# Optimization experiments

Hardware: AMD Instinct MI355X
Metric: run time of the kernel (lower is better)

Reference implementation:

```python
import jax, jax.numpy as jnp
import numpy as np

# Production-scale perfect decision-tree ensemble (Hummingbird perf_tree_trav layout)
B, F, T, D, C = 16384, 256, 512, 7, 4  # batch, features, trees, internal levels below root, classes


def setup_inputs() -> dict:
    key = jax.random.key(0)
    k = jax.random.split(key, 6)
    total = T * (2 ** (D + 1) - 2)  # concatenated per-level node/bias tables, level l has T*2^l entries
    return {
        "x": jax.random.normal(k[0], (B, F), dtype=jnp.float32),
        "root_nodes": jax.random.randint(k[1], (T,), 0, F, dtype=jnp.int32),
        "root_biases": jax.random.normal(k[2], (T,), dtype=jnp.float32),
        "tree_indices": jnp.arange(T, dtype=jnp.int32) * 2,
        "nodes_flat": jax.random.randint(k[3], (total,), 0, F, dtype=jnp.int32),
        "biases_flat": jax.random.normal(k[4], (total,), dtype=jnp.float32),
        "leaf_nodes": jax.random.normal(k[5], (T * 2 ** (D + 1), C), dtype=jnp.float32),
    }


def reference(x, root_nodes, root_biases, tree_indices, nodes_flat, biases_flat, leaf_nodes):
    # Root level: compare each tree's root feature against its bias. decision_cond = less (lt).
    # tree_indices = t*2 offsets indices into the flat level-1 table of size 2T;
    # the offset doubles along with the level size via `2*idx + cond`.
    idx = (x[:, root_nodes] < root_biases).astype(jnp.int32) + tree_indices  # [B, T]
    off = 0
    for l in range(1, D + 1):  # static loop over tree depth
        size = T << l
        lvl_nodes = nodes_flat[off:off + size]
        lvl_biases = biases_flat[off:off + size]
        feat_idx = lvl_nodes[idx]                          # [B, T] feature ids for current nodes
        feats = jnp.take_along_axis(x, feat_idx, axis=1)   # [B, T] per-sample feature gather
        idx = 2 * idx + (feats < lvl_biases[idx]).astype(jnp.int32)
        off += size
    leaves = leaf_nodes[idx]                               # [B, T, C]
    return leaves.sum(axis=1)                              # [B, C]
```

## Files before the change

### kernel.cpp

```cpp
#include <hip/hip_runtime.h>

#define BB 16384
#define FF 256
#define TT 512
#define DD 7

constexpr int S_  = 64;
constexpr int NT_ = 1024;
constexpr int NTG = NT_ / S_;
constexpr int HT  = TT / 2;
constexpr int TPT = HT / NTG;
constexpr int NP  = 8;
constexpr int NJ  = TPT / NP;

constexpr int NR1 = TT * 2;
constexpr int NR3 = TT * 8;
constexpr int NR5 = TT * 32;
constexpr int NN7 = TT * 128;
constexpr int NRECS = NR1 + NR3 + NR5 + NN7;

constexpr size_t OFF_R3   = (size_t)NR1 * 16;
constexpr size_t OFF_R5   = OFF_R3 + (size_t)NR3 * 16;
constexpr size_t OFF_N7   = OFF_R5 + (size_t)NR5 * 16;
constexpr size_t OFF_PART = OFF_N7 + (size_t)NN7 * 8;
constexpr size_t WS_NEED  = OFF_PART + (size_t)2 * BB * 4 * sizeof(float);

__global__ void pack_kernel(const int* __restrict__ nf, const float* __restrict__ bf,
                            int4* __restrict__ R1, int4* __restrict__ R3,
                            int4* __restrict__ R5, int2* __restrict__ N7) {
    const int i = blockIdx.x * 256 + threadIdx.x;
    if (i < NR1) {
        const int e0 = i, eC = 2 * TT + 2 * i;
        const int fp = (nf[e0] & 255) | ((nf[eC] & 255) << 8) | ((nf[eC + 1] & 255) << 16);
        R1[i] = make_int4(fp, __float_as_int(bf[e0]),
                          __float_as_int(bf[eC]), __float_as_int(bf[eC + 1]));
    } else if (i < NR1 + NR3) {
        const int r = i - NR1;
        const int e0 = 6 * TT + r, eC = 14 * TT + 2 * r;
        const int fp = (nf[e0] & 255) | ((nf[eC] & 255) << 8) | ((nf[eC + 1] & 255) << 16);
        R3[r] = make_int4(fp, __float_as_int(bf[e0]),
                          __float_as_int(bf[eC]), __float_as_int(bf[eC + 1]));
    } else if (i < NR1 + NR3 + NR5) {
        const int r = i - NR1 - NR3;
        const int e0 = 30 * TT + r, eC = 62 * TT + 2 * r;
        const int fp = (nf[e0] & 255) | ((nf[eC] & 255) << 8) | ((nf[eC + 1] & 255) << 16);
        R5[r] = make_int4(fp, __float_as_int(bf[e0]),
                          __float_as_int(bf[eC]), __float_as_int(bf[eC + 1]));
    } else if (i < NRECS) {
        const int r = i - NR1 - NR3 - NR5;
        const int e = 126 * TT + r;
        N7[r] = make_int2(nf[e], __float_as_int(bf[e]));
    }
}

__device__ __forceinline__ int step2(const int4 w, const int i,
                                     const float* __restrict__ x_s,
                                     const int xb, const int sz) {
    const float v0 = x_s[xb | ((w.x & 255) ^ sz)];
    const float vL = x_s[xb | (((w.x >> 8) & 255) ^ sz)];
    const float vR = x_s[xb | (((w.x >> 16) & 255) ^ sz)];
    const int   c0 = (v0 < __int_as_float(w.y)) ? 1 : 0;
    const float vc = c0 ? vR : vL;
    const float bc = c0 ? __int_as_float(w.w) : __int_as_float(w.z);
    const int   c1 = (vc < bc) ? 1 : 0;
    return 4 * i + 2 * c0 + c1;
}

__global__ __launch_bounds__(NT_, 8)
void tree_traverse_kernel(const float* __restrict__ x,
                          const int*   __restrict__ root_nodes,
                          const float* __restrict__ root_biases,
                          const float4* __restrict__ leaf4,
                          const int4*  __restrict__ R1, const int4* __restrict__ R3,
                          const int4*  __restrict__ R5, const int2* __restrict__ N7,
                          float*       __restrict__ part)
{
    extern __shared__ float x_s[];

    const int tid = threadIdx.x;
    const int s   = tid & (S_ - 1);
    const int tg  = tid >> 6;
    const int s0  = blockIdx.x * S_;
    const int h0  = blockIdx.y * HT;

    {
        const float4* xg = (const float4*)(x + (size_t)s0 * FF);
        const int r  = tid >> 4;
        const int v  = tid & 15;
        const int rz = r & 31;
        float* row = x_s + (r << 8);
        #pragma unroll
        for (int c = 0; c < 4; ++c) {
            const float4 q = xg[r * (FF / 4) + v + 16 * c];
            const int f0 = (v + 16 * c) * 4;
            row[(f0 + 0) ^ rz] = q.x;
            row[(f0 + 1) ^ rz] = q.y;
            row[(f0 + 2) ^ rz] = q.z;
            row[(f0 + 3) ^ rz] = q.w;
        }
    }
    __syncthreads();

    const int xb = s << 8;
    const int sz = s & 31;
    float a0 = 0.f, a1 = 0.f, a2 = 0.f, a3 = 0.f;

    #pragma unroll 1
    for (int j = 0; j < NJ; ++j) {
        const int tbase = h0 + tg * TPT + j * NP;
        int p[NP];

        #pragma unroll
        for (int k = 0; k < NP; ++k) {
            const int t = tbase + k;
            p[k] = (x_s[xb | (root_nodes[t] ^ sz)] < root_biases[t]) ? 1 : 0;
        }
        #pragma unroll
        for (int k = 0; k < NP; ++k)
            p[k] = step2(R1[((tbase + k) << 1) + p[k]], p[k], x_s, xb, sz);
        #pragma unroll
        for (int k = 0; k < NP; ++k)
            p[k] = step2(R3[((tbase + k) << 3) + p[k]], p[k], x_s, xb, sz);
        #pragma unroll
        for (int k = 0; k < NP; ++k)
            p[k] = step2(R5[((tbase + k) << 5) + p[k]], p[k], x_s, xb, sz);
        #pragma unroll
        for (int k = 0; k < NP; ++k) {
            const int2 n = N7[((tbase + k) << 7) + p[k]];
            const int c = (x_s[xb | ((n.x & 255) ^ sz)] < __int_as_float(n.y)) ? 1 : 0;
            p[k] = 2 * p[k] + c;
        }
        #pragma unroll
        for (int k = 0; k < NP; ++k) {
            const float4 lf = leaf4[((tbase + k) << 8) + p[k]];
            a0 += lf.x; a1 += lf.y; a2 += lf.z; a3 += lf.w;
        }
    }

    __syncthreads();
    ((float4*)x_s)[tid] = make_float4(a0, a1, a2, a3);
    __syncthreads();
    if (tid < S_ * 4) {
        float o = 0.f;
        #pragma unroll
        for (int g = 0; g < NTG; ++g)
            o += x_s[(g << 8) + tid];
        part[((size_t)blockIdx.y * BB + s0) * 4 + tid] = o;
    }
}

__global__ void sum_kernel(const float4* __restrict__ part, float4* __restrict__ out) {
    const int i = blockIdx.x * 256 + threadIdx.x;
    if (i < BB) {
        const float4 a = part[i], b = part[BB + i];
        out[i] = make_float4(a.x + b.x, a.y + b.y, a.z + b.z, a.w + b.w);
    }
}

__global__ __launch_bounds__(NT_, 4)
void tree_traverse_fallback(const float* __restrict__ x,
                            const int* __restrict__ root_nodes,
                            const float* __restrict__ root_biases,
                            const int* __restrict__ nodes_flat,
                            const float* __restrict__ biases_flat,
                            const float* __restrict__ leaf_nodes,
                            float* __restrict__ out)
{
    extern __shared__ float x_s[];
    const int tid = threadIdx.x;
    const int s = tid & (S_ - 1), tg = tid >> 6;
    const int s0 = blockIdx.x * S_;
    {
        const float4* xg = (const float4*)(x + (size_t)s0 * FF);
        const int r = tid >> 4, v = tid & 15, rz = r & 31;
        float* row = x_s + (r << 8);
        #pragma unroll
        for (int c = 0; c < 4; ++c) {
            const float4 q = xg[r * (FF / 4) + v + 16 * c];
            const int f0 = (v + 16 * c) * 4;
            row[(f0 + 0) ^ rz] = q.x; row[(f0 + 1) ^ rz] = q.y;
            row[(f0 + 2) ^ rz] = q.z; row[(f0 + 3) ^ rz] = q.w;
        }
    }
    __syncthreads();
    const int xb = s << 8, sz = s & 31;
    const float4* leaf4 = (const float4*)leaf_nodes;
    float a0 = 0.f, a1 = 0.f, a2 = 0.f, a3 = 0.f;
    #pragma unroll 1
    for (int j = 0; j < TT / NTG / NP; ++j) {
        const int tbase = tg * (TT / NTG) + j * NP;
        int p[NP];
        #pragma unroll
        for (int k = 0; k < NP; ++k) {
            const int t = tbase + k;
            p[k] = 2 * t + ((x_s[xb | (root_nodes[t] ^ sz)] < root_biases[t]) ? 1 : 0);
        }
        #pragma unroll
        for (int l = 1; l <= DD; ++l) {
            #pragma unroll
            for (int k = 0; k < NP; ++k) {
                const int fi = nodes_flat[p[k]];
                const float bi = biases_flat[p[k]];
                const int c = (x_s[xb | (fi ^ sz)] < bi) ? 1 : 0;
                p[k] = 2 * p[k] + 2 * TT + c;
            }
        }
        #pragma unroll
        for (int k = 0; k < NP; ++k) {
            const float4 lf = leaf4[p[k] - 254 * TT];
            a0 += lf.x; a1 += lf.y; a2 += lf.z; a3 += lf.w;
        }
    }
    __syncthreads();
    ((float4*)x_s)[tid] = make_float4(a0, a1, a2, a3);
    __syncthreads();
    if (tid < S_ * 4) {
        float o = 0.f;
        #pragma unroll
        for (int g = 0; g < NTG; ++g) o += x_s[(g << 8) + tid];
        out[(size_t)s0 * 4 + tid] = o;
    }
}

extern "C" void kernel_launch(void* const* d_in, const int* in_sizes, int n_in,
                              void* d_out, int out_size, void* d_ws, size_t ws_size,
                              hipStream_t stream) {
    const float* x           = (const float*)d_in[0];
    const int*   root_nodes  = (const int*)  d_in[1];
    const float* root_biases = (const float*)d_in[2];
    const int*   nodes_flat  = (const int*)  d_in[4];
    const float* biases_flat = (const float*)d_in[5];
    const float* leaf_nodes  = (const float*)d_in[6];
    float*       out         = (float*)d_out;

    constexpr size_t LDS_BYTES = (size_t)S_ * FF * sizeof(float);

    if (ws_size >= WS_NEED) {
        char* ws = (char*)d_ws;
        int4* R1 = (int4*)ws;
        int4* R3 = (int4*)(ws + OFF_R3);
        int4* R5 = (int4*)(ws + OFF_R5);
        int2* N7 = (int2*)(ws + OFF_N7);
        float* part = (float*)(ws + OFF_PART);

        pack_kernel<<<(NRECS + 255) / 256, 256, 0, stream>>>(
            nodes_flat, biases_flat, R1, R3, R5, N7);
        dim3 grid(BB / S_, 2);
        tree_traverse_kernel<<<grid, NT_, LDS_BYTES, stream>>>(
            x, root_nodes, root_biases, (const float4*)leaf_nodes,
            R1, R3, R5, N7, part);
        sum_kernel<<<BB / 256, 256, 0, stream>>>((const float4*)part, (float4*)out);
    } else {
        tree_traverse_fallback<<<BB / S_, NT_, LDS_BYTES, stream>>>(
            x, root_nodes, root_biases, nodes_flat, biases_flat, leaf_nodes, out);
    }
}
```

Baseline: 108.9 us.

## Prefetch fp16 leaf pairs with level-7 nodes and hoist uniform root-level loads

Packs each pair of sibling leaves as fp16 into a 16-byte record indexed by the level-7 node, so the leaf values load together with the last node record instead of after its comparison. The root and level-1 step now loads both level-1 candidates with wave-uniform addresses and selects in registers, removing a dependent gather. This shortens the chain of dependent memory accesses per tree. The cost is fp16 rounding of leaf values, plus an extra packing pass over the leaf table.

```diff
diff --git a/kernel.cpp b/kernel.cpp
--- a/kernel.cpp
+++ b/kernel.cpp
@@ -1,4 +1,5 @@
 #include <hip/hip_runtime.h>
+#include <hip/hip_fp16.h>
 
 #define BB 16384
 #define FF 256
@@ -17,17 +18,20 @@
 constexpr int NR3 = TT * 8;
 constexpr int NR5 = TT * 32;
 constexpr int NN7 = TT * 128;
-constexpr int NRECS = NR1 + NR3 + NR5 + NN7;
+constexpr int NTOT = NR1 + NR3 + NR5 + NN7 + NN7;
 
 constexpr size_t OFF_R3   = (size_t)NR1 * 16;
 constexpr size_t OFF_R5   = OFF_R3 + (size_t)NR3 * 16;
 constexpr size_t OFF_N7   = OFF_R5 + (size_t)NR5 * 16;
-constexpr size_t OFF_PART = OFF_N7 + (size_t)NN7 * 8;
+constexpr size_t OFF_LP   = OFF_N7 + (size_t)NN7 * 8;
+constexpr size_t OFF_PART = OFF_LP + (size_t)NN7 * 16;
 constexpr size_t WS_NEED  = OFF_PART + (size_t)2 * BB * 4 * sizeof(float);
 
 __global__ void pack_kernel(const int* __restrict__ nf, const float* __restrict__ bf,
+                            const float4* __restrict__ leaf4,
                             int4* __restrict__ R1, int4* __restrict__ R3,
-                            int4* __restrict__ R5, int2* __restrict__ N7) {
+                            int4* __restrict__ R5, int2* __restrict__ N7,
+                            uint4* __restrict__ LP) {
     const int i = blockIdx.x * 256 + threadIdx.x;
     if (i < NR1) {
         const int e0 = i, eC = 2 * TT + 2 * i;
@@ -46,10 +50,21 @@
         const int fp = (nf[e0] & 255) | ((nf[eC] & 255) << 8) | ((nf[eC + 1] & 255) << 16);
         R5[r] = make_int4(fp, __float_as_int(bf[e0]),
                           __float_as_int(bf[eC]), __float_as_int(bf[eC + 1]));
-    } else if (i < NRECS) {
+    } else if (i < NR1 + NR3 + NR5 + NN7) {
         const int r = i - NR1 - NR3 - NR5;
         const int e = 126 * TT + r;
-        N7[r] = make_int2(nf[e], __float_as_int(bf[e]));
+        N7[r] = make_int2(nf[e] & 255, __float_as_int(bf[e]));
+    } else if (i < NTOT) {
+        const int j = i - NR1 - NR3 - NR5 - NN7;
+        const float4 l0 = leaf4[2 * j], l1 = leaf4[2 * j + 1];
+        const __half2 a = __floats2half2_rn(l0.x, l0.y), b = __floats2half2_rn(l0.z, l0.w);
+        const __half2 c = __floats2half2_rn(l1.x, l1.y), d = __floats2half2_rn(l1.z, l1.w);
+        uint4 w;
+        w.x = *reinterpret_cast<const unsigned int*>(&a);
+        w.y = *reinterpret_cast<const unsigned int*>(&b);
+        w.z = *reinterpret_cast<const unsigned int*>(&c);
+        w.w = *reinterpret_cast<const unsigned int*>(&d);
+        LP[j] = w;
     }
 }
 
@@ -70,9 +85,9 @@
 void tree_traverse_kernel(const float* __restrict__ x,
                           const int*   __restrict__ root_nodes,
                           const float* __restrict__ root_biases,
-                          const float4* __restrict__ leaf4,
                           const int4*  __restrict__ R1, const int4* __restrict__ R3,
                           const int4*  __restrict__ R5, const int2* __restrict__ N7,
+                          const uint4* __restrict__ LP,
                           float*       __restrict__ part)
 {
     extern __shared__ float x_s[];
@@ -112,12 +127,17 @@
 
         #pragma unroll
         for (int k = 0; k < NP; ++k) {
-            const int t = tbase + k;
-            p[k] = (x_s[xb | (root_nodes[t] ^ sz)] < root_biases[t]) ? 1 : 0;
-        }
-        #pragma unroll
-        for (int k = 0; k < NP; ++k)
-            p[k] = step2(R1[((tbase + k) << 1) + p[k]], p[k], x_s, xb, sz);
+            const int tu = __builtin_amdgcn_readfirstlane(tbase + k);
+            const int   rn  = root_nodes[tu];
+            const float rbv = root_biases[tu];
+            const int4  rA  = R1[2 * tu];
+            const int4  rB  = R1[2 * tu + 1];
+            const int c0 = (x_s[xb | (rn ^ sz)] < rbv) ? 1 : 0;
+            int4 r;
+            r.x = c0 ? rB.x : rA.x;  r.y = c0 ? rB.y : rA.y;
+            r.z = c0 ? rB.z : rA.z;  r.w = c0 ? rB.w : rA.w;
+            p[k] = step2(r, c0, x_s, xb, sz);
+        }
         #pragma unroll
         for (int k = 0; k < NP; ++k)
             p[k] = step2(R3[((tbase + k) << 3) + p[k]], p[k], x_s, xb, sz);
@@ -126,14 +146,15 @@
             p[k] = step2(R5[((tbase + k) << 5) + p[k]], p[k], x_s, xb, sz);
         #pragma unroll
         for (int k = 0; k < NP; ++k) {
-            const int2 n = N7[((tbase + k) << 7) + p[k]];
-            const int c = (x_s[xb | ((n.x & 255) ^ sz)] < __int_as_float(n.y)) ? 1 : 0;
-            p[k] = 2 * p[k] + c;
-        }
-        #pragma unroll
-        for (int k = 0; k < NP; ++k) {
-            const float4 lf = leaf4[((tbase + k) << 8) + p[k]];
-            a0 += lf.x; a1 += lf.y; a2 += lf.z; a3 += lf.w;
+            const int idx7 = ((tbase + k) << 7) + p[k];
+            const int2  n  = N7[idx7];
+            const uint4 lp = LP[idx7];
+            const int c7 = (x_s[xb | (n.x ^ sz)] < __int_as_float(n.y)) ? 1 : 0;
+            const unsigned int w01 = c7 ? lp.z : lp.x;
+            const unsigned int w23 = c7 ? lp.w : lp.y;
+            const float2 f01 = __half22float2(*reinterpret_cast<const __half2*>(&w01));
+            const float2 f23 = __half22float2(*reinterpret_cast<const __half2*>(&w23));
+            a0 += f01.x; a1 += f01.y; a2 += f23.x; a3 += f23.y;
         }
     }
 
@@ -237,18 +258,18 @@
 
     if (ws_size >= WS_NEED) {
         char* ws = (char*)d_ws;
-        int4* R1 = (int4*)ws;
-        int4* R3 = (int4*)(ws + OFF_R3);
-        int4* R5 = (int4*)(ws + OFF_R5);
-        int2* N7 = (int2*)(ws + OFF_N7);
+        int4*  R1 = (int4*)ws;
+        int4*  R3 = (int4*)(ws + OFF_R3);
+        int4*  R5 = (int4*)(ws + OFF_R5);
+        int2*  N7 = (int2*)(ws + OFF_N7);
+        uint4* LP = (uint4*)(ws + OFF_LP);
         float* part = (float*)(ws + OFF_PART);
 
-        pack_kernel<<<(NRECS + 255) / 256, 256, 0, stream>>>(
-            nodes_flat, biases_flat, R1, R3, R5, N7);
+        pack_kernel<<<(NTOT + 255) / 256, 256, 0, stream>>>(
+            nodes_flat, biases_flat, (const float4*)leaf_nodes, R1, R3, R5, N7, LP);
         dim3 grid(BB / S_, 2);
         tree_traverse_kernel<<<grid, NT_, LDS_BYTES, stream>>>(
-            x, root_nodes, root_biases, (const float4*)leaf_nodes,
-            R1, R3, R5, N7, part);
+            x, root_nodes, root_biases, R1, R3, R5, N7, LP, part);
         sum_kernel<<<BB / 256, 256, 0, stream>>>((const float4*)part, (float4*)out);
     } else {
         tree_traverse_fallback<<<BB / S_, NT_, LDS_BYTES, stream>>>(
```

Result: faster. 102.8 us (-5.6%).
